# Performance work log

Measured on AMD Instinct MI355X. Metric: run time of the kernel, lower is better.

## Reference

```python
import jax, jax.numpy as jnp
import numpy as np

LN_EPS = 1e-6

def hsigmoid(v):
    # HSigmoid with bias=3, divisor=6: clamp((v+3)/6, 0, 1)
    return jnp.clip((v + 3.0) / 6.0, 0.0, 1.0)

def setup_inputs() -> dict:
    key = jax.random.key(0)
    ks = jax.random.split(key, 10)
    b, c, h, w = 8, 512, 64, 64
    s = lambda fan: 1.0 / np.sqrt(fan)
    return {
        "x": jax.random.normal(ks[0], (b, c, h, w), jnp.float32),
        "w_b1": jax.random.normal(ks[1], (c // 2, c), jnp.float32) * s(c),
        "b_b1": jax.random.normal(ks[2], (c // 2,), jnp.float32) * 0.01,
        "w_b2": jax.random.normal(ks[3], (c, c // 2), jnp.float32) * s(c // 2),
        "b_b2": jax.random.normal(ks[4], (c,), jnp.float32) * 0.01,
        "w_conv1": jax.random.normal(ks[5], (1, c), jnp.float32) * s(c),
        "ln_g": jnp.ones((c,), jnp.float32),
        "ln_b": jnp.zeros((c,), jnp.float32),
        "sk_w1": jax.random.normal(ks[6], (c // 2, c), jnp.float32) * s(c),
        "sk_w2": jax.random.normal(ks[7], (c, c // 2), jnp.float32) * s(c // 2),
        "res_w": jax.random.normal(ks[8], (c, c), jnp.float32) * s(c),
    }

def reference(x, w_b1, b_b1, w_b2, b_b2, w_conv1, ln_g, ln_b, sk_w1, sk_w2, res_w):
    b, c, h, w = x.shape
    # --- channel attention: GAP -> 1x1 conv+ReLU -> 1x1 conv+HSigmoid -> LN over c ---
    g = x.mean(axis=(2, 3))                                  # (b, c)
    ca = jax.nn.relu(g @ w_b1.T + b_b1)                      # (b, c/2)
    ca = hsigmoid(ca @ w_b2.T + b_b2)                        # (b, c)
    mu = ca.mean(axis=-1, keepdims=True)
    var = ca.var(axis=-1, keepdims=True)
    ca = (ca - mu) / jnp.sqrt(var + LN_EPS) * ln_g + ln_b    # LayerNorm over channels
    channel_attn = ca[:, :, None, None]                      # (b, c, 1, 1)
    # --- spatial attention: 1x1 conv (c->1, no bias) + HSigmoid ---
    spatial_attn = hsigmoid(jnp.einsum('bchw,c->bhw', x, w_conv1[0]))[:, None]  # (b,1,h,w)
    # --- parallel attention: torch float // 2 == floor((a+b)/2) ---
    par_attn = jnp.floor((spatial_attn + channel_attn) / 2.0)  # (b, c, h, w)
    # --- sequence attention: bmm outer product (b,c,1)x(b,1,hw) ---
    seq_attn = channel_attn * spatial_attn                     # (b, c, h, w)
    # --- SK module: GAP(sum) -> conv+ReLU -> conv+ReLU -> softmax over c ---
    u = (seq_attn + par_attn).mean(axis=(2, 3))                # (b, c)
    u = jax.nn.relu(u @ sk_w1.T)
    u = jax.nn.relu(u @ sk_w2.T)
    a = jax.nn.softmax(u, axis=1)[:, :, None, None]            # (b, c, 1, 1)
    selected_attn = seq_attn * a + par_attn * (1.0 - a)        # (b, c, h, w)
    # --- self attention: spatial sum + 1x1 residual conv ---
    self_attn = selected_attn.sum(axis=(2, 3))[:, :, None, None] \
        + jnp.einsum('bchw,oc->bohw', x, res_w)                # (b, c, h, w)
    return x * selected_attn + self_attn
```

## Files before the change

kernel.cpp:

```cpp
#include <hip/hip_runtime.h>
#include <stdint.h>

#define HW 4096
#define NC 512
#define NB 8

typedef __attribute__((ext_vector_type(8))) short short8;
typedef __attribute__((ext_vector_type(4))) float f32x4;

__device__ __forceinline__ unsigned short f2bf(float f) {
  unsigned int u = __builtin_bit_cast(unsigned int, f);
  unsigned int r = (u + 0x7FFFu + ((u >> 16) & 1u)) >> 16;
  return (unsigned short)r;
}
__device__ __forceinline__ float hsig(float v) {
  return fminf(fmaxf((v + 3.0f) * (1.0f / 6.0f), 0.0f), 1.0f);
}

__device__ __forceinline__ void gload16(const void* g, void* l) {
  __builtin_amdgcn_global_load_lds(
      (const __attribute__((address_space(1))) unsigned int*)g,
      (__attribute__((address_space(3))) unsigned int*)l, 16, 0, 0);
}

__device__ __forceinline__ float wave_reduce(float p) {
#pragma unroll
  for (int m = 1; m < 64; m <<= 1) p += __shfl_xor(p, m);
  return p;
}

__device__ __forceinline__ float block_reduce_sum(float v, volatile float* red) {
  int t = threadIdx.x;
#pragma unroll
  for (int m = 1; m < 64; m <<= 1) v += __shfl_xor(v, m);
  if ((t & 63) == 0) red[t >> 6] = v;
  __syncthreads();
  v = red[0] + red[1] + red[2] + red[3];
  __syncthreads();
  return v;
}
__device__ __forceinline__ float block_reduce_max(float v, volatile float* red) {
  int t = threadIdx.x;
#pragma unroll
  for (int m = 1; m < 64; m <<= 1) v = fmaxf(v, __shfl_xor(v, m));
  if ((t & 63) == 0) red[t >> 6] = v;
  __syncthreads();
  v = fmaxf(fmaxf(red[0], red[1]), fmaxf(red[2], red[3]));
  __syncthreads();
  return v;
}

__global__ __launch_bounds__(256) void k1_stats_transpose(
    const float* __restrict__ x, const float* __restrict__ w_conv1,
    const float* __restrict__ res_w,
    float* __restrict__ g_sum, float* __restrict__ spat,
    unsigned short* __restrict__ xTS, unsigned short* __restrict__ wbfS) {
  __shared__ float sp_lds[16][64];
  __shared__ unsigned short t_lds[64 * 72];
  const int t = threadIdx.x;
  const int b = blockIdx.z;
  const int c0 = blockIdx.y * 64;
  const int h0 = blockIdx.x * 64;
  const int cg = t >> 4;
  const int hg = t & 15;

  float vv[4][4];
  float wc[4];
  const float* xb = x + ((size_t)(b * NC + c0 + cg * 4) * HW) + h0 + hg * 4;
#pragma unroll
  for (int i = 0; i < 4; i++) {
    float4 v = *(const float4*)(xb + (size_t)i * HW);
    vv[i][0] = v.x; vv[i][1] = v.y; vv[i][2] = v.z; vv[i][3] = v.w;
    wc[i] = w_conv1[c0 + cg * 4 + i];
  }
#pragma unroll
  for (int i = 0; i < 4; i++) {
    float s = vv[i][0] + vv[i][1] + vv[i][2] + vv[i][3];
    s += __shfl_xor(s, 1); s += __shfl_xor(s, 2);
    s += __shfl_xor(s, 4); s += __shfl_xor(s, 8);
    if (hg == 0) atomicAdd(&g_sum[b * NC + c0 + cg * 4 + i], s);
  }
  {
    float4 sp;
    sp.x = vv[0][0] * wc[0] + vv[1][0] * wc[1] + vv[2][0] * wc[2] + vv[3][0] * wc[3];
    sp.y = vv[0][1] * wc[0] + vv[1][1] * wc[1] + vv[2][1] * wc[2] + vv[3][1] * wc[3];
    sp.z = vv[0][2] * wc[0] + vv[1][2] * wc[1] + vv[2][2] * wc[2] + vv[3][2] * wc[3];
    sp.w = vv[0][3] * wc[0] + vv[1][3] * wc[1] + vv[2][3] * wc[2] + vv[3][3] * wc[3];
    *(float4*)&sp_lds[cg][hg * 4] = sp;
  }
#pragma unroll
  for (int j = 0; j < 4; j++) {
    ushort4 u;
    u.x = f2bf(vv[0][j]); u.y = f2bf(vv[1][j]);
    u.z = f2bf(vv[2][j]); u.w = f2bf(vv[3][j]);
    *(ushort4*)&t_lds[(hg * 4 + j) * 72 + cg * 4] = u;
  }
  __syncthreads();
  if (t < 64) {
    float s = 0.f;
#pragma unroll
    for (int i = 0; i < 16; i++) s += sp_lds[i][t];
    atomicAdd(&spat[b * HW + h0 + t], s);
  }
  const int w = t >> 6, l = t & 63;
#pragma unroll
  for (int ff = w; ff < 8; ff += 4) {
    const int fr = ff >> 1, fk = ff & 1;
    short8 v = *(const short8*)&t_lds[(fr * 16 + (l & 15)) * 72 + (fk * 4 + (l >> 4)) * 8];
    size_t tile = (size_t)(b * 256 + (h0 >> 4) + fr) * 16 + (c0 >> 5) + fk;
    *(short8*)(xTS + tile * 512 + l * 8) = v;
  }
  if (b == 0 && t < 64) {
    const int q = blockIdx.y * 64 + blockIdx.x;
    float4 a = *(const float4*)(res_w + (size_t)q * 512 + t * 8);
    float4 c2 = *(const float4*)(res_w + (size_t)q * 512 + t * 8 + 4);
    short8 v;
    v[0] = (short)f2bf(a.x); v[1] = (short)f2bf(a.y);
    v[2] = (short)f2bf(a.z); v[3] = (short)f2bf(a.w);
    v[4] = (short)f2bf(c2.x); v[5] = (short)f2bf(c2.y);
    v[6] = (short)f2bf(c2.z); v[7] = (short)f2bf(c2.w);
    const int lq = (q & 15) + ((t & 3) << 4);
    *(short8*)(wbfS + ((size_t)(q >> 4) * 16 + (t >> 2)) * 512 + lq * 8) = v;
  }
}


__global__ __launch_bounds__(256) void k2_mv1(
    const float* __restrict__ g_sum, const float* __restrict__ spat,
    const float* __restrict__ w_b1, const float* __restrict__ b_b1,
    float* __restrict__ s_out, float* __restrict__ Ssum,
    float* __restrict__ ca1) {
  const int l = threadIdx.x & 63;
  const int W = blockIdx.x * 4 + (threadIdx.x >> 6);
  const int b = W >> 8, o = W & 255;
  const float* wr = w_b1 + (size_t)o * 512 + l * 8;
  float4 wa = *(const float4*)wr;
  float4 wb = *(const float4*)(wr + 4);
  const float* gr = g_sum + b * NC + l * 8;
  float4 ga = *(const float4*)gr;
  float4 gb = *(const float4*)(gr + 4);
  float p = wa.x * ga.x + wa.y * ga.y + wa.z * ga.z + wa.w * ga.w +
            wb.x * gb.x + wb.y * gb.y + wb.z * gb.z + wb.w * gb.w;
  p = wave_reduce(p);
  if (l == 0) ca1[b * 256 + o] = fmaxf(p * (1.0f / 4096.0f) + b_b1[o], 0.0f);
  if (blockIdx.x < 32) {
    const int b2 = blockIdx.x >> 2;
    const int i4 = (blockIdx.x & 3) * 256 + threadIdx.x;
    float4 v = ((const float4*)(spat + (size_t)b2 * HW))[i4];
    float4 os;
    os.x = hsig(v.x); os.y = hsig(v.y); os.z = hsig(v.z); os.w = hsig(v.w);
    ((float4*)(s_out + (size_t)b2 * HW))[i4] = os;
    float sum = wave_reduce(os.x + os.y + os.z + os.w);
    if (l == 0) atomicAdd(&Ssum[b2], sum);
  }
}

__global__ __launch_bounds__(256) void k2_mv2(
    const float* __restrict__ ca1, const float* __restrict__ w_b2,
    const float* __restrict__ b_b2, float* __restrict__ ca2) {
  const int l = threadIdx.x & 63;
  const int W = blockIdx.x * 4 + (threadIdx.x >> 6);
  const int b = W >> 9, o = W & 511;
  float4 wv = ((const float4*)(w_b2 + (size_t)o * 256))[l];
  float4 cv = ((const float4*)(ca1 + b * 256))[l];
  float p = wv.x * cv.x + wv.y * cv.y + wv.z * cv.z + wv.w * cv.w;
  p = wave_reduce(p);
  if (l == 0) ca2[b * NC + o] = hsig(p + b_b2[o]);
}

__global__ __launch_bounds__(256) void k2_ln(
    const float* __restrict__ ca2, const float* __restrict__ ln_g,
    const float* __restrict__ ln_b, float* __restrict__ t_out) {
  __shared__ float red[4];
  const int b = blockIdx.x, t = threadIdx.x;
  float v0 = ca2[b * NC + t], v1 = ca2[b * NC + t + 256];
  float S = block_reduce_sum(v0 + v1, red);
  float SQ = block_reduce_sum(v0 * v0 + v1 * v1, red);
  float mu = S * (1.0f / 512.0f);
  float var = SQ * (1.0f / 512.0f) - mu * mu;
  float rstd = rsqrtf(var + 1e-6f);
  t_out[b * NC + t] = (v0 - mu) * rstd * ln_g[t] + ln_b[t];
  t_out[b * NC + t + 256] = (v1 - mu) * rstd * ln_g[t + 256] + ln_b[t + 256];
}

__global__ __launch_bounds__(256) void k2b_floorsum(
    const float* __restrict__ s, const float* __restrict__ t_arr, float* __restrict__ P) {
  __shared__ float s_l[4096];
  const int t = threadIdx.x;
  const int b = blockIdx.y;
  const int c0 = blockIdx.x * 16;
  const float* sb = s + b * HW;
#pragma unroll
  for (int i = 0; i < 16; i++) s_l[t + i * 256] = sb[t + i * 256];
  __syncthreads();
  const int w = t >> 6, l = t & 63;
#pragma unroll
  for (int j = 0; j < 4; j++) {
    int c = c0 + w * 4 + j;
    float tc = t_arr[b * NC + c];
    float sum = 0.f;
#pragma unroll 8
    for (int i = 0; i < 64; i++) sum += floorf((s_l[l + i * 64] + tc) * 0.5f);
#pragma unroll
    for (int m = 1; m < 64; m <<= 1) sum += __shfl_xor(sum, m);
    if (l == 0) P[b * NC + c] = sum;
  }
}

__global__ __launch_bounds__(256) void k2_sk1(
    const float* __restrict__ t_arr, const float* __restrict__ P,
    const float* __restrict__ Ssum, const float* __restrict__ sk_w1,
    float* __restrict__ u1) {
  const int l = threadIdx.x & 63;
  const int W = blockIdx.x * 4 + (threadIdx.x >> 6);
  const int b = W >> 8, o = W & 255;
  const float Ss = Ssum[b];
  const float* wr = sk_w1 + (size_t)o * 512 + l * 8;
  float4 wa = *(const float4*)wr;
  float4 wb = *(const float4*)(wr + 4);
  const float* tr = t_arr + b * NC + l * 8;
  const float* pr = P + b * NC + l * 8;
  float4 ta = *(const float4*)tr, tb = *(const float4*)(tr + 4);
  float4 Pa = *(const float4*)pr, Pb = *(const float4*)(pr + 4);
  float4 ua, ub;
  ua.x = ta.x * Ss + Pa.x; ua.y = ta.y * Ss + Pa.y;
  ua.z = ta.z * Ss + Pa.z; ua.w = ta.w * Ss + Pa.w;
  ub.x = tb.x * Ss + Pb.x; ub.y = tb.y * Ss + Pb.y;
  ub.z = tb.z * Ss + Pb.z; ub.w = tb.w * Ss + Pb.w;
  float p = wa.x * ua.x + wa.y * ua.y + wa.z * ua.z + wa.w * ua.w +
            wb.x * ub.x + wb.y * ub.y + wb.z * ub.z + wb.w * ub.w;
  p = wave_reduce(p) * (1.0f / 4096.0f);
  if (l == 0) u1[b * 256 + o] = fmaxf(p, 0.0f);
}

__global__ __launch_bounds__(256) void k2_sk2(
    const float* __restrict__ u1, const float* __restrict__ sk_w2,
    float* __restrict__ u2) {
  const int l = threadIdx.x & 63;
  const int W = blockIdx.x * 4 + (threadIdx.x >> 6);
  const int b = W >> 9, o = W & 511;
  float4 wv = ((const float4*)(sk_w2 + (size_t)o * 256))[l];
  float4 cv = ((const float4*)(u1 + b * 256))[l];
  float p = wv.x * cv.x + wv.y * cv.y + wv.z * cv.z + wv.w * cv.w;
  p = wave_reduce(p);
  if (l == 0) u2[b * NC + o] = fmaxf(p, 0.0f);
}

__global__ __launch_bounds__(256) void k2_smx(
    const float* __restrict__ u2, const float* __restrict__ t_arr,
    const float* __restrict__ P, const float* __restrict__ Ssum,
    float* __restrict__ coef) {
  __shared__ float red[4];
  const int b = blockIdx.x, t = threadIdx.x;
  const float Ss = Ssum[b];
  float v0 = u2[b * NC + t], v1 = u2[b * NC + t + 256];
  float M = block_reduce_max(fmaxf(v0, v1), red);
  float e0 = __expf(v0 - M), e1 = __expf(v1 - M);
  float Z = block_reduce_sum(e0 + e1, red);
  float inv = 1.0f / Z;
#pragma unroll
  for (int h = 0; h < 2; h++) {
    int o = t + h * 256;
    float a = (h == 0 ? e0 : e1) * inv;
    float tc = t_arr[b * NC + o];
    float Pv = P[b * NC + o];
    float c1 = a * tc;
    float c2 = 1.0f - a;
    float c3 = c1 * Ss + c2 * Pv;
    float4 cf = {c1, c2, c3, tc};
    *(float4*)(coef + (size_t)(b * NC + o) * 4) = cf;
  }
}

__global__ __launch_bounds__(256, 4) void k3_gemm_epilogue(
    const unsigned short* __restrict__ wbfS, const unsigned short* __restrict__ xTS,
    const float* __restrict__ x, const float* __restrict__ s,
    const float* __restrict__ coef, float* __restrict__ out) {
  __shared__ __align__(16) char smem[32768];
  const int t = threadIdx.x;
  const int bx = blockIdx.x, mz = blockIdx.y, b = blockIdx.z;
  const int w = t >> 6, l = t & 63;
  const int wm = w >> 1, wn = w & 1;
  const int l16 = l & 15, quad = l >> 4;

  f32x4 acc[4][4];
#pragma unroll
  for (int mi = 0; mi < 4; mi++)
#pragma unroll
    for (int ni = 0; ni < 4; ni++) {
      f32x4 z = {0.f, 0.f, 0.f, 0.f};
      acc[mi][ni] = z;
    }

  const char* gA0 = (const char*)wbfS + ((size_t)(mz * 8 + 2 * w) * 16) * 1024 + l * 16;
  const char* gA1 = gA0 + 16 * 1024;
  const char* gB0 = (const char*)xTS + ((size_t)(b * 256 + bx * 8 + 2 * w) * 16) * 1024 + l * 16;
  const char* gB1 = gB0 + 16 * 1024;
  char* lA0 = smem + (2 * w) * 1024;
  char* lA1 = smem + (2 * w + 1) * 1024;
  char* lB0 = smem + 8192 + (2 * w) * 1024;
  char* lB1 = smem + 8192 + (2 * w + 1) * 1024;
  const char* pA = smem + wm * 4096 + l * 16;
  const char* pB = smem + 8192 + wn * 4096 + l * 16;

#define K3_STAGE(buf, kk) do {                                  \
    gload16(gA0 + (kk) * 1024, lA0 + (buf) * 16384);            \
    gload16(gA1 + (kk) * 1024, lA1 + (buf) * 16384);            \
    gload16(gB0 + (kk) * 1024, lB0 + (buf) * 16384);            \
    gload16(gB1 + (kk) * 1024, lB1 + (buf) * 16384);            \
  } while (0)

#define K3_COMPUTE(buf) do {                                    \
    short8 af[4], bfr[4];                                       \
    _Pragma("unroll")                                           \
    for (int mi = 0; mi < 4; mi++)                              \
      af[mi] = *(const short8*)(pA + (buf) * 16384 + mi * 1024);\
    _Pragma("unroll")                                           \
    for (int ni = 0; ni < 4; ni++)                              \
      bfr[ni] = *(const short8*)(pB + (buf) * 16384 + ni * 1024);\
    _Pragma("unroll")                                           \
    for (int mi = 0; mi < 4; mi++)                              \
      _Pragma("unroll")                                         \
      for (int ni = 0; ni < 4; ni++)                            \
        acc[mi][ni] = __builtin_amdgcn_mfma_f32_16x16x32_bf16(  \
            af[mi], bfr[ni], acc[mi][ni], 0, 0, 0);             \
  } while (0)

  K3_STAGE(0, 0);
  __syncthreads();
#pragma unroll
  for (int kk = 0; kk < 16; kk += 2) {
    K3_STAGE(1, kk + 1);
    K3_COMPUTE(0);
    __syncthreads();
    if (kk + 2 < 16) K3_STAGE(0, kk + 2);
    K3_COMPUTE(1);
    __syncthreads();
  }

  float* eb = (float*)smem + w * 1088;
  const int row = l >> 2, cb = (l & 3) * 16;
  const int colb = bx * 128 + wn * 64 + cb;
  const float* sp = s + b * HW + colb;
  float4 sv[4];
#pragma unroll
  for (int j = 0; j < 4; j++) sv[j] = *(const float4*)(sp + 4 * j);
#pragma unroll
  for (int mi = 0; mi < 4; mi++) {
#pragma unroll
    for (int ni = 0; ni < 4; ni++)
#pragma unroll
      for (int r = 0; r < 4; r++)
        eb[(quad * 4 + r) * 68 + ni * 16 + l16] = acc[mi][ni][r];
    const int o = mz * 128 + wm * 64 + mi * 16 + row;
    float4 cf = *(const float4*)(coef + (size_t)(b * NC + o) * 4);
    const size_t rbase = (size_t)(b * NC + o) * HW + colb;
#pragma unroll
    for (int j = 0; j < 4; j++) {
      f32x4 y = *(f32x4*)&eb[row * 68 + cb + 4 * j];
      float4 svj = sv[j];
      float4 xv = *(const float4*)(x + rbase + 4 * j);
      float4 ov;
      ov.x = xv.x * (cf.x * svj.x + cf.y * floorf((svj.x + cf.w) * 0.5f)) + cf.z + y.x;
      ov.y = xv.y * (cf.x * svj.y + cf.y * floorf((svj.y + cf.w) * 0.5f)) + cf.z + y.y;
      ov.z = xv.z * (cf.x * svj.z + cf.y * floorf((svj.z + cf.w) * 0.5f)) + cf.z + y.z;
      ov.w = xv.w * (cf.x * svj.w + cf.y * floorf((svj.w + cf.w) * 0.5f)) + cf.z + y.w;
      *(float4*)(out + rbase + 4 * j) = ov;
    }
  }
#undef K3_STAGE
#undef K3_COMPUTE
}

extern "C" void kernel_launch(void* const* d_in, const int* in_sizes, int n_in,
                              void* d_out, int out_size, void* d_ws, size_t ws_size,
                              hipStream_t stream) {
  const float* x       = (const float*)d_in[0];
  const float* w_b1    = (const float*)d_in[1];
  const float* b_b1    = (const float*)d_in[2];
  const float* w_b2    = (const float*)d_in[3];
  const float* b_b2    = (const float*)d_in[4];
  const float* w_conv1 = (const float*)d_in[5];
  const float* ln_g    = (const float*)d_in[6];
  const float* ln_b    = (const float*)d_in[7];
  const float* sk_w1   = (const float*)d_in[8];
  const float* sk_w2   = (const float*)d_in[9];
  const float* res_w   = (const float*)d_in[10];
  float* out = (float*)d_out;
  char* ws = (char*)d_ws;

  float* g_sum = (float*)(ws + 0x00000);
  float* spat  = (float*)(ws + 0x08000);
  float* Ssum  = (float*)(ws + 0x28000);
  float* t_arr = (float*)(ws + 0x29000);
  float* P     = (float*)(ws + 0x30000);
  float* coef  = (float*)(ws + 0x38000);
  float* s     = (float*)(ws + 0x50000);
  float* ca1   = (float*)(ws + 0x70000);
  float* u1    = (float*)(ws + 0x72000);
  float* ca2   = (float*)(ws + 0x74000);
  float* u2    = (float*)(ws + 0x78000);
  unsigned short* wbfS = (unsigned short*)(ws + 0x80000);
  unsigned short* xTS  = (unsigned short*)(ws + 0x100000);

  hipMemsetAsync(ws, 0, 0x28040, stream);
  k1_stats_transpose<<<dim3(64, 8, 8), 256, 0, stream>>>(x, w_conv1, res_w, g_sum, spat, xTS, wbfS);
  k2_mv1<<<512, 256, 0, stream>>>(g_sum, spat, w_b1, b_b1, s, Ssum, ca1);
  k2_mv2<<<1024, 256, 0, stream>>>(ca1, w_b2, b_b2, ca2);
  k2_ln<<<8, 256, 0, stream>>>(ca2, ln_g, ln_b, t_arr);
  k2b_floorsum<<<dim3(32, 8), 256, 0, stream>>>(s, t_arr, P);
  k2_sk1<<<512, 256, 0, stream>>>(t_arr, P, Ssum, sk_w1, u1);
  k2_sk2<<<1024, 256, 0, stream>>>(u1, sk_w2, u2);
  k2_smx<<<8, 256, 0, stream>>>(u2, t_arr, P, Ssum, coef);
  k3_gemm_epilogue<<<dim3(32, 4, 8), 256, 0, stream>>>(wbfS, xTS, x, s, coef, out);
}
```

Measured before the change: 196.0 us.

## Fuse seven small attention-vector kernels into one cooperative kernel with grid syncs

Replaces the chain of seven tiny launches (two matvecs, LayerNorm, floor-sum, two SK matvecs, softmax) with a single cooperative kernel of 512 blocks that separates the stages with grid.sync(). The aim is to remove per-launch overhead and inter-kernel gaps on a latency-bound chain of small vector ops. Work per stage is remapped so that 512 blocks cover each stage, with some waves doing two outputs. In exchange it adds grid-wide barrier cost and requires all 512 blocks, each with 16KB shared memory, to be co-resident.

New measurement: 508.4 us. 159% more time.

```diff
diff --git a/kernel.cpp b/kernel.cpp
--- a/kernel.cpp
+++ b/kernel.cpp
@@ -1,5 +1,8 @@
 #include <hip/hip_runtime.h>
+#include <hip/hip_cooperative_groups.h>
 #include <stdint.h>
+
+namespace cg = cooperative_groups;
 
 #define HW 4096
 #define NC 512
@@ -124,28 +127,40 @@
   }
 }
 
-
-__global__ __launch_bounds__(256) void k2_mv1(
+__global__ __launch_bounds__(256) void k2_coop(
     const float* __restrict__ g_sum, const float* __restrict__ spat,
     const float* __restrict__ w_b1, const float* __restrict__ b_b1,
+    const float* __restrict__ w_b2, const float* __restrict__ b_b2,
+    const float* __restrict__ ln_g, const float* __restrict__ ln_b,
+    const float* __restrict__ sk_w1, const float* __restrict__ sk_w2,
     float* __restrict__ s_out, float* __restrict__ Ssum,
-    float* __restrict__ ca1) {
-  const int l = threadIdx.x & 63;
-  const int W = blockIdx.x * 4 + (threadIdx.x >> 6);
-  const int b = W >> 8, o = W & 255;
-  const float* wr = w_b1 + (size_t)o * 512 + l * 8;
-  float4 wa = *(const float4*)wr;
-  float4 wb = *(const float4*)(wr + 4);
-  const float* gr = g_sum + b * NC + l * 8;
-  float4 ga = *(const float4*)gr;
-  float4 gb = *(const float4*)(gr + 4);
-  float p = wa.x * ga.x + wa.y * ga.y + wa.z * ga.z + wa.w * ga.w +
-            wb.x * gb.x + wb.y * gb.y + wb.z * gb.z + wb.w * gb.w;
-  p = wave_reduce(p);
-  if (l == 0) ca1[b * 256 + o] = fmaxf(p * (1.0f / 4096.0f) + b_b1[o], 0.0f);
-  if (blockIdx.x < 32) {
-    const int b2 = blockIdx.x >> 2;
-    const int i4 = (blockIdx.x & 3) * 256 + threadIdx.x;
+    float* __restrict__ ca1, float* __restrict__ ca2,
+    float* __restrict__ t_arr, float* __restrict__ P,
+    float* __restrict__ u1, float* __restrict__ u2,
+    float* __restrict__ coef) {
+  __shared__ float s_l[4096];
+  __shared__ float red[4];
+  cg::grid_group grid = cg::this_grid();
+  const int t = threadIdx.x, blk = blockIdx.x;
+  const int l = t & 63;
+  const int Wv = blk * 4 + (t >> 6);
+
+  {
+    const int b = Wv >> 8, o = Wv & 255;
+    const float* wr = w_b1 + (size_t)o * 512 + l * 8;
+    float4 wa = *(const float4*)wr;
+    float4 wb = *(const float4*)(wr + 4);
+    const float* gr = g_sum + b * NC + l * 8;
+    float4 ga = *(const float4*)gr;
+    float4 gb = *(const float4*)(gr + 4);
+    float p = wa.x * ga.x + wa.y * ga.y + wa.z * ga.z + wa.w * ga.w +
+              wb.x * gb.x + wb.y * gb.y + wb.z * gb.z + wb.w * gb.w;
+    p = wave_reduce(p);
+    if (l == 0) ca1[b * 256 + o] = fmaxf(p * (1.0f / 4096.0f) + b_b1[o], 0.0f);
+  }
+  if (blk < 32) {
+    const int b2 = blk >> 2;
+    const int i4 = (blk & 3) * 256 + t;
     float4 v = ((const float4*)(spat + (size_t)b2 * HW))[i4];
     float4 os;
     os.x = hsig(v.x); os.y = hsig(v.y); os.z = hsig(v.z); os.w = hsig(v.w);
@@ -153,122 +168,111 @@
     float sum = wave_reduce(os.x + os.y + os.z + os.w);
     if (l == 0) atomicAdd(&Ssum[b2], sum);
   }
-}
-
-__global__ __launch_bounds__(256) void k2_mv2(
-    const float* __restrict__ ca1, const float* __restrict__ w_b2,
-    const float* __restrict__ b_b2, float* __restrict__ ca2) {
-  const int l = threadIdx.x & 63;
-  const int W = blockIdx.x * 4 + (threadIdx.x >> 6);
-  const int b = W >> 9, o = W & 511;
-  float4 wv = ((const float4*)(w_b2 + (size_t)o * 256))[l];
-  float4 cv = ((const float4*)(ca1 + b * 256))[l];
-  float p = wv.x * cv.x + wv.y * cv.y + wv.z * cv.z + wv.w * cv.w;
-  p = wave_reduce(p);
-  if (l == 0) ca2[b * NC + o] = hsig(p + b_b2[o]);
-}
-
-__global__ __launch_bounds__(256) void k2_ln(
-    const float* __restrict__ ca2, const float* __restrict__ ln_g,
-    const float* __restrict__ ln_b, float* __restrict__ t_out) {
-  __shared__ float red[4];
-  const int b = blockIdx.x, t = threadIdx.x;
-  float v0 = ca2[b * NC + t], v1 = ca2[b * NC + t + 256];
-  float S = block_reduce_sum(v0 + v1, red);
-  float SQ = block_reduce_sum(v0 * v0 + v1 * v1, red);
-  float mu = S * (1.0f / 512.0f);
-  float var = SQ * (1.0f / 512.0f) - mu * mu;
-  float rstd = rsqrtf(var + 1e-6f);
-  t_out[b * NC + t] = (v0 - mu) * rstd * ln_g[t] + ln_b[t];
-  t_out[b * NC + t + 256] = (v1 - mu) * rstd * ln_g[t + 256] + ln_b[t + 256];
-}
-
-__global__ __launch_bounds__(256) void k2b_floorsum(
-    const float* __restrict__ s, const float* __restrict__ t_arr, float* __restrict__ P) {
-  __shared__ float s_l[4096];
-  const int t = threadIdx.x;
-  const int b = blockIdx.y;
-  const int c0 = blockIdx.x * 16;
-  const float* sb = s + b * HW;
-#pragma unroll
-  for (int i = 0; i < 16; i++) s_l[t + i * 256] = sb[t + i * 256];
-  __syncthreads();
-  const int w = t >> 6, l = t & 63;
-#pragma unroll
-  for (int j = 0; j < 4; j++) {
-    int c = c0 + w * 4 + j;
-    float tc = t_arr[b * NC + c];
-    float sum = 0.f;
+  grid.sync();
+
+  {
+    const int b = Wv >> 8, ob = Wv & 255;
+    float4 cv = ((const float4*)(ca1 + b * 256))[l];
+#pragma unroll
+    for (int h = 0; h < 2; h++) {
+      const int o = ob + h * 256;
+      float4 wv = ((const float4*)(w_b2 + (size_t)o * 256))[l];
+      float p = wv.x * cv.x + wv.y * cv.y + wv.z * cv.z + wv.w * cv.w;
+      p = wave_reduce(p);
+      if (l == 0) ca2[b * NC + o] = hsig(p + b_b2[o]);
+    }
+  }
+  grid.sync();
+
+  if (blk < 8) {
+    const int b = blk;
+    float v0 = ca2[b * NC + t], v1 = ca2[b * NC + t + 256];
+    float S = block_reduce_sum(v0 + v1, red);
+    float SQ = block_reduce_sum(v0 * v0 + v1 * v1, red);
+    float mu = S * (1.0f / 512.0f);
+    float var = SQ * (1.0f / 512.0f) - mu * mu;
+    float rstd = rsqrtf(var + 1e-6f);
+    t_arr[b * NC + t] = (v0 - mu) * rstd * ln_g[t] + ln_b[t];
+    t_arr[b * NC + t + 256] = (v1 - mu) * rstd * ln_g[t + 256] + ln_b[t + 256];
+  }
+  grid.sync();
+
+  {
+    const int b = blk >> 6, cg2 = blk & 63;
+    const float* sb = s_out + (size_t)b * HW;
+#pragma unroll
+    for (int i = 0; i < 16; i++) s_l[t + i * 256] = sb[t + i * 256];
+    __syncthreads();
+    const int w = t >> 6;
+#pragma unroll
+    for (int j = 0; j < 2; j++) {
+      const int c = cg2 * 8 + w * 2 + j;
+      const float tc = t_arr[b * NC + c];
+      float sum = 0.f;
 #pragma unroll 8
-    for (int i = 0; i < 64; i++) sum += floorf((s_l[l + i * 64] + tc) * 0.5f);
-#pragma unroll
-    for (int m = 1; m < 64; m <<= 1) sum += __shfl_xor(sum, m);
-    if (l == 0) P[b * NC + c] = sum;
-  }
-}
-
-__global__ __launch_bounds__(256) void k2_sk1(
-    const float* __restrict__ t_arr, const float* __restrict__ P,
-    const float* __restrict__ Ssum, const float* __restrict__ sk_w1,
-    float* __restrict__ u1) {
-  const int l = threadIdx.x & 63;
-  const int W = blockIdx.x * 4 + (threadIdx.x >> 6);
-  const int b = W >> 8, o = W & 255;
-  const float Ss = Ssum[b];
-  const float* wr = sk_w1 + (size_t)o * 512 + l * 8;
-  float4 wa = *(const float4*)wr;
-  float4 wb = *(const float4*)(wr + 4);
-  const float* tr = t_arr + b * NC + l * 8;
-  const float* pr = P + b * NC + l * 8;
-  float4 ta = *(const float4*)tr, tb = *(const float4*)(tr + 4);
-  float4 Pa = *(const float4*)pr, Pb = *(const float4*)(pr + 4);
-  float4 ua, ub;
-  ua.x = ta.x * Ss + Pa.x; ua.y = ta.y * Ss + Pa.y;
-  ua.z = ta.z * Ss + Pa.z; ua.w = ta.w * Ss + Pa.w;
-  ub.x = tb.x * Ss + Pb.x; ub.y = tb.y * Ss + Pb.y;
-  ub.z = tb.z * Ss + Pb.z; ub.w = tb.w * Ss + Pb.w;
-  float p = wa.x * ua.x + wa.y * ua.y + wa.z * ua.z + wa.w * ua.w +
-            wb.x * ub.x + wb.y * ub.y + wb.z * ub.z + wb.w * ub.w;
-  p = wave_reduce(p) * (1.0f / 4096.0f);
-  if (l == 0) u1[b * 256 + o] = fmaxf(p, 0.0f);
-}
-
-__global__ __launch_bounds__(256) void k2_sk2(
-    const float* __restrict__ u1, const float* __restrict__ sk_w2,
-    float* __restrict__ u2) {
-  const int l = threadIdx.x & 63;
-  const int W = blockIdx.x * 4 + (threadIdx.x >> 6);
-  const int b = W >> 9, o = W & 511;
-  float4 wv = ((const float4*)(sk_w2 + (size_t)o * 256))[l];
-  float4 cv = ((const float4*)(u1 + b * 256))[l];
-  float p = wv.x * cv.x + wv.y * cv.y + wv.z * cv.z + wv.w * cv.w;
-  p = wave_reduce(p);
-  if (l == 0) u2[b * NC + o] = fmaxf(p, 0.0f);
-}
-
-__global__ __launch_bounds__(256) void k2_smx(
-    const float* __restrict__ u2, const float* __restrict__ t_arr,
-    const float* __restrict__ P, const float* __restrict__ Ssum,
-    float* __restrict__ coef) {
-  __shared__ float red[4];
-  const int b = blockIdx.x, t = threadIdx.x;
-  const float Ss = Ssum[b];
-  float v0 = u2[b * NC + t], v1 = u2[b * NC + t + 256];
-  float M = block_reduce_max(fmaxf(v0, v1), red);
-  float e0 = __expf(v0 - M), e1 = __expf(v1 - M);
-  float Z = block_reduce_sum(e0 + e1, red);
-  float inv = 1.0f / Z;
-#pragma unroll
-  for (int h = 0; h < 2; h++) {
-    int o = t + h * 256;
-    float a = (h == 0 ? e0 : e1) * inv;
-    float tc = t_arr[b * NC + o];
-    float Pv = P[b * NC + o];
-    float c1 = a * tc;
-    float c2 = 1.0f - a;
-    float c3 = c1 * Ss + c2 * Pv;
-    float4 cf = {c1, c2, c3, tc};
-    *(float4*)(coef + (size_t)(b * NC + o) * 4) = cf;
+      for (int i = 0; i < 64; i++) sum += floorf((s_l[l + i * 64] + tc) * 0.5f);
+      sum = wave_reduce(sum);
+      if (l == 0) P[b * NC + c] = sum;
+    }
+  }
+  grid.sync();
+
+  {
+    const int b = Wv >> 8, o = Wv & 255;
+    const float Ss = Ssum[b];
+    const float* wr = sk_w1 + (size_t)o * 512 + l * 8;
+    float4 wa = *(const float4*)wr;
+    float4 wb = *(const float4*)(wr + 4);
+    const float* tr = t_arr + b * NC + l * 8;
+    const float* pr = P + b * NC + l * 8;
+    float4 ta = *(const float4*)tr, tb = *(const float4*)(tr + 4);
+    float4 Pa = *(const float4*)pr, Pb = *(const float4*)(pr + 4);
+    float4 ua, ub;
+    ua.x = ta.x * Ss + Pa.x; ua.y = ta.y * Ss + Pa.y;
+    ua.z = ta.z * Ss + Pa.z; ua.w = ta.w * Ss + Pa.w;
+    ub.x = tb.x * Ss + Pb.x; ub.y = tb.y * Ss + Pb.y;
+    ub.z = tb.z * Ss + Pb.z; ub.w = tb.w * Ss + Pb.w;
+    float p = wa.x * ua.x + wa.y * ua.y + wa.z * ua.z + wa.w * ua.w +
+              wb.x * ub.x + wb.y * ub.y + wb.z * ub.z + wb.w * ub.w;
+    p = wave_reduce(p) * (1.0f / 4096.0f);
+    if (l == 0) u1[b * 256 + o] = fmaxf(p, 0.0f);
+  }
+  grid.sync();
+
+  {
+    const int b = Wv >> 8, ob = Wv & 255;
+    float4 cv = ((const float4*)(u1 + b * 256))[l];
+#pragma unroll
+    for (int h = 0; h < 2; h++) {
+      const int o = ob + h * 256;
+      float4 wv = ((const float4*)(sk_w2 + (size_t)o * 256))[l];
+      float p = wv.x * cv.x + wv.y * cv.y + wv.z * cv.z + wv.w * cv.w;
+      p = wave_reduce(p);
+      if (l == 0) u2[b * NC + o] = fmaxf(p, 0.0f);
+    }
+  }
+  grid.sync();
+
+  if (blk < 8) {
+    const int b = blk;
+    const float Ss = Ssum[b];
+    float v0 = u2[b * NC + t], v1 = u2[b * NC + t + 256];
+    float M = block_reduce_max(fmaxf(v0, v1), red);
+    float e0 = __expf(v0 - M), e1 = __expf(v1 - M);
+    float Z = block_reduce_sum(e0 + e1, red);
+    float inv = 1.0f / Z;
+#pragma unroll
+    for (int h = 0; h < 2; h++) {
+      const int o = t + h * 256;
+      float a = (h == 0 ? e0 : e1) * inv;
+      float tc = t_arr[b * NC + o];
+      float Pv = P[b * NC + o];
+      float c1 = a * tc;
+      float c2 = 1.0f - a;
+      float c3 = c1 * Ss + c2 * Pv;
+      float4 cf = {c1, c2, c3, tc};
+      *(float4*)(coef + (size_t)(b * NC + o) * 4) = cf;
+    }
   }
 }
 
@@ -405,12 +409,13 @@
 
   hipMemsetAsync(ws, 0, 0x28040, stream);
   k1_stats_transpose<<<dim3(64, 8, 8), 256, 0, stream>>>(x, w_conv1, res_w, g_sum, spat, xTS, wbfS);
-  k2_mv1<<<512, 256, 0, stream>>>(g_sum, spat, w_b1, b_b1, s, Ssum, ca1);
-  k2_mv2<<<1024, 256, 0, stream>>>(ca1, w_b2, b_b2, ca2);
-  k2_ln<<<8, 256, 0, stream>>>(ca2, ln_g, ln_b, t_arr);
-  k2b_floorsum<<<dim3(32, 8), 256, 0, stream>>>(s, t_arr, P);
-  k2_sk1<<<512, 256, 0, stream>>>(t_arr, P, Ssum, sk_w1, u1);
-  k2_sk2<<<1024, 256, 0, stream>>>(u1, sk_w2, u2);
-  k2_smx<<<8, 256, 0, stream>>>(u2, t_arr, P, Ssum, coef);
+  {
+    void* args[] = {(void*)&g_sum, (void*)&spat, (void*)&w_b1, (void*)&b_b1,
+                    (void*)&w_b2, (void*)&b_b2, (void*)&ln_g, (void*)&ln_b,
+                    (void*)&sk_w1, (void*)&sk_w2, (void*)&s, (void*)&Ssum,
+                    (void*)&ca1, (void*)&ca2, (void*)&t_arr, (void*)&P,
+                    (void*)&u1, (void*)&u2, (void*)&coef};
+    hipLaunchCooperativeKernel((void*)k2_coop, dim3(512), dim3(256), args, 0, stream);
+  }
   k3_gemm_epilogue<<<dim3(32, 4, 8), 256, 0, stream>>>(wbfS, xTS, x, s, coef, out);
 }
```

## Fuse LayerNorm into floorsum and softmax into GEMM prologue to cut launches

Applied to the files above, without the earlier changes.

Folds the LayerNorm kernel into the floor-sum kernel, so each block recomputes the per-batch LN statistics and derives its channel values directly. The softmax and coefficient computation move into the GEMM kernel's prologue, and the coefficients are kept in shared memory instead of a global buffer. This removes two tiny serial launches and their global round trips. In exchange, the LN and softmax reductions are recomputed redundantly in every block, and the GEMM kernel uses a little more shared memory. The floor-sum kernel relies on the block reductions' barriers to cover the shared-memory fill of s_l.

New measurement: 194.0 us. Within noise of the previous version (-1.0%).

```diff
diff --git a/kernel.cpp b/kernel.cpp
--- a/kernel.cpp
+++ b/kernel.cpp
@@ -168,36 +168,30 @@
   if (l == 0) ca2[b * NC + o] = hsig(p + b_b2[o]);
 }
 
-__global__ __launch_bounds__(256) void k2_ln(
-    const float* __restrict__ ca2, const float* __restrict__ ln_g,
-    const float* __restrict__ ln_b, float* __restrict__ t_out) {
+__global__ __launch_bounds__(256) void k2b_floorsum_ln(
+    const float* __restrict__ s, const float* __restrict__ ca2,
+    const float* __restrict__ ln_g, const float* __restrict__ ln_b,
+    float* __restrict__ t_arr, float* __restrict__ P) {
+  __shared__ float s_l[4096];
   __shared__ float red[4];
-  const int b = blockIdx.x, t = threadIdx.x;
+  const int t = threadIdx.x;
+  const int b = blockIdx.y;
+  const int c0 = blockIdx.x * 16;
+  const float* sb = s + b * HW;
+#pragma unroll
+  for (int i = 0; i < 16; i++) s_l[t + i * 256] = sb[t + i * 256];
   float v0 = ca2[b * NC + t], v1 = ca2[b * NC + t + 256];
   float S = block_reduce_sum(v0 + v1, red);
   float SQ = block_reduce_sum(v0 * v0 + v1 * v1, red);
   float mu = S * (1.0f / 512.0f);
   float var = SQ * (1.0f / 512.0f) - mu * mu;
   float rstd = rsqrtf(var + 1e-6f);
-  t_out[b * NC + t] = (v0 - mu) * rstd * ln_g[t] + ln_b[t];
-  t_out[b * NC + t + 256] = (v1 - mu) * rstd * ln_g[t + 256] + ln_b[t + 256];
-}
-
-__global__ __launch_bounds__(256) void k2b_floorsum(
-    const float* __restrict__ s, const float* __restrict__ t_arr, float* __restrict__ P) {
-  __shared__ float s_l[4096];
-  const int t = threadIdx.x;
-  const int b = blockIdx.y;
-  const int c0 = blockIdx.x * 16;
-  const float* sb = s + b * HW;
-#pragma unroll
-  for (int i = 0; i < 16; i++) s_l[t + i * 256] = sb[t + i * 256];
-  __syncthreads();
   const int w = t >> 6, l = t & 63;
 #pragma unroll
   for (int j = 0; j < 4; j++) {
     int c = c0 + w * 4 + j;
-    float tc = t_arr[b * NC + c];
+    float tc = (ca2[b * NC + c] - mu) * rstd * ln_g[c] + ln_b[c];
+    if (l == 0) t_arr[b * NC + c] = tc;
     float sum = 0.f;
 #pragma unroll 8
     for (int i = 0; i < 64; i++) sum += floorf((s_l[l + i * 64] + tc) * 0.5f);
@@ -246,42 +240,40 @@
   if (l == 0) u2[b * NC + o] = fmaxf(p, 0.0f);
 }
 
-__global__ __launch_bounds__(256) void k2_smx(
-    const float* __restrict__ u2, const float* __restrict__ t_arr,
-    const float* __restrict__ P, const float* __restrict__ Ssum,
-    float* __restrict__ coef) {
-  __shared__ float red[4];
-  const int b = blockIdx.x, t = threadIdx.x;
-  const float Ss = Ssum[b];
-  float v0 = u2[b * NC + t], v1 = u2[b * NC + t + 256];
-  float M = block_reduce_max(fmaxf(v0, v1), red);
-  float e0 = __expf(v0 - M), e1 = __expf(v1 - M);
-  float Z = block_reduce_sum(e0 + e1, red);
-  float inv = 1.0f / Z;
-#pragma unroll
-  for (int h = 0; h < 2; h++) {
-    int o = t + h * 256;
-    float a = (h == 0 ? e0 : e1) * inv;
-    float tc = t_arr[b * NC + o];
-    float Pv = P[b * NC + o];
-    float c1 = a * tc;
-    float c2 = 1.0f - a;
-    float c3 = c1 * Ss + c2 * Pv;
-    float4 cf = {c1, c2, c3, tc};
-    *(float4*)(coef + (size_t)(b * NC + o) * 4) = cf;
-  }
-}
-
 __global__ __launch_bounds__(256, 4) void k3_gemm_epilogue(
     const unsigned short* __restrict__ wbfS, const unsigned short* __restrict__ xTS,
     const float* __restrict__ x, const float* __restrict__ s,
-    const float* __restrict__ coef, float* __restrict__ out) {
-  __shared__ __align__(16) char smem[32768];
+    const float* __restrict__ u2, const float* __restrict__ t_arr,
+    const float* __restrict__ P, const float* __restrict__ Ssum,
+    float* __restrict__ out) {
+  __shared__ __align__(16) char smem[34816];
+  __shared__ float red4[4];
   const int t = threadIdx.x;
   const int bx = blockIdx.x, mz = blockIdx.y, b = blockIdx.z;
   const int w = t >> 6, l = t & 63;
   const int wm = w >> 1, wn = w & 1;
   const int l16 = l & 15, quad = l >> 4;
+
+  float4* cf_l = (float4*)(smem + 32768);
+  {
+    const float Ss = Ssum[b];
+    float v0 = u2[b * NC + t], v1 = u2[b * NC + t + 256];
+    float M = block_reduce_max(fmaxf(v0, v1), red4);
+    float e0 = __expf(v0 - M), e1 = __expf(v1 - M);
+    float Z = block_reduce_sum(e0 + e1, red4);
+    float inv = 1.0f / Z;
+    if (t < 128) {
+      const int o = mz * 128 + t;
+      float a = __expf(u2[b * NC + o] - M) * inv;
+      float tc = t_arr[b * NC + o];
+      float Pv = P[b * NC + o];
+      float c1 = a * tc;
+      float c2v = 1.0f - a;
+      float c3 = c1 * Ss + c2v * Pv;
+      float4 cf = {c1, c2v, c3, tc};
+      cf_l[t] = cf;
+    }
+  }
 
   f32x4 acc[4][4];
 #pragma unroll
@@ -353,7 +345,7 @@
       for (int r = 0; r < 4; r++)
         eb[(quad * 4 + r) * 68 + ni * 16 + l16] = acc[mi][ni][r];
     const int o = mz * 128 + wm * 64 + mi * 16 + row;
-    float4 cf = *(const float4*)(coef + (size_t)(b * NC + o) * 4);
+    float4 cf = cf_l[wm * 64 + mi * 16 + row];
     const size_t rbase = (size_t)(b * NC + o) * HW + colb;
 #pragma unroll
     for (int j = 0; j < 4; j++) {
@@ -394,7 +386,6 @@
   float* Ssum  = (float*)(ws + 0x28000);
   float* t_arr = (float*)(ws + 0x29000);
   float* P     = (float*)(ws + 0x30000);
-  float* coef  = (float*)(ws + 0x38000);
   float* s     = (float*)(ws + 0x50000);
   float* ca1   = (float*)(ws + 0x70000);
   float* u1    = (float*)(ws + 0x72000);
@@ -407,10 +398,8 @@
   k1_stats_transpose<<<dim3(64, 8, 8), 256, 0, stream>>>(x, w_conv1, res_w, g_sum, spat, xTS, wbfS);
   k2_mv1<<<512, 256, 0, stream>>>(g_sum, spat, w_b1, b_b1, s, Ssum, ca1);
   k2_mv2<<<1024, 256, 0, stream>>>(ca1, w_b2, b_b2, ca2);
-  k2_ln<<<8, 256, 0, stream>>>(ca2, ln_g, ln_b, t_arr);
-  k2b_floorsum<<<dim3(32, 8), 256, 0, stream>>>(s, t_arr, P);
+  k2b_floorsum_ln<<<dim3(32, 8), 256, 0, stream>>>(s, ca2, ln_g, ln_b, t_arr, P);
   k2_sk1<<<512, 256, 0, stream>>>(t_arr, P, Ssum, sk_w1, u1);
   k2_sk2<<<1024, 256, 0, stream>>>(u1, sk_w2, u2);
-  k2_smx<<<8, 256, 0, stream>>>(u2, t_arr, P, Ssum, coef);
-  k3_gemm_epilogue<<<dim3(32, 4, 8), 256, 0, stream>>>(wbfS, xTS, x, s, coef, out);
-}
+  k3_gemm_epilogue<<<dim3(32, 4, 8), 256, 0, stream>>>(wbfS, xTS, x, s, u2, t_arr, P, Ssum, out);
+}
```
